# Kernel tuning notes

Measured on AMD Instinct MI355X. Metric: run time of the kernel, lower is better.

The kernel has to match this reference:

```python
import jax, jax.numpy as jnp
import numpy as np

B, S, D_IN, D_H, D_OUT = 32, 1024, 512, 512, 512
N_HEADS, K_NEI = 2, 3
LN_EPS = 1e-5


def _layernorm(x, g, b):
    mu = x.mean(-1, keepdims=True)
    xc = x - mu
    var = (xc * xc).mean(-1, keepdims=True)
    return xc * jax.lax.rsqrt(var + LN_EPS) * g + b


def setup_inputs() -> dict:
    key = jax.random.key(0)
    ks = jax.random.split(key, 8)
    sc = 0.02
    rn = lambda k, shape: jax.random.normal(k, shape, jnp.float32) * sc
    return {
        "x": jax.random.normal(ks[0], (B, S, D_IN), jnp.float32),
        "enc_w": rn(ks[1], (D_H, D_IN)), "enc_b": jnp.zeros((D_H,), jnp.float32),
        "in_w": rn(ks[2], (3 * D_H, D_H)), "in_b": jnp.zeros((3 * D_H,), jnp.float32),
        "out_w": rn(ks[3], (D_H, D_H)), "out_b": jnp.zeros((D_H,), jnp.float32),
        "ln1_g": jnp.ones((D_H,), jnp.float32), "ln1_b": jnp.zeros((D_H,), jnp.float32),
        "ffn_w1": rn(ks[4], (2 * D_H, D_H)), "ffn_b1": jnp.zeros((2 * D_H,), jnp.float32),
        "ffn_w2": rn(ks[5], (D_H, 2 * D_H)), "ffn_b2": jnp.zeros((D_H,), jnp.float32),
        "gc_w": rn(ks[6], (D_H, 2 * D_H)), "gc_b": jnp.zeros((D_H,), jnp.float32),
        "ln2_g": jnp.ones((D_H,), jnp.float32), "ln2_b": jnp.zeros((D_H,), jnp.float32),
        "dec_w": rn(ks[7], (D_OUT, D_H)), "dec_b": jnp.zeros((D_OUT,), jnp.float32),
    }


def reference(x, enc_w, enc_b, in_w, in_b, out_w, out_b, ln1_g, ln1_b,
              ffn_w1, ffn_b1, ffn_w2, ffn_b2, gc_w, gc_b, ln2_g, ln2_b,
              dec_w, dec_b):
    # --- encoder ---
    h = jax.nn.relu(x @ enc_w.T + enc_b)                          # [B,S,Dh]

    # --- ElevateH0toH1: self-attention + LN + residual FFN ---
    qkv = h @ in_w.T + in_b                                       # [B,S,3Dh]
    q, k, v = jnp.split(qkv, 3, axis=-1)
    dh = D_H // N_HEADS
    heads = lambda t: t.reshape(B, S, N_HEADS, dh).transpose(0, 2, 1, 3)
    q, k, v = heads(q), heads(k), heads(v)
    scores = jnp.einsum("bhqd,bhkd->bhqk", q, k) / jnp.sqrt(jnp.float32(dh))
    attn = jax.nn.softmax(scores, axis=-1)
    ctx = jnp.einsum("bhqk,bhkd->bhqd", attn, v)
    ctx = ctx.transpose(0, 2, 1, 3).reshape(B, S, D_H)
    attn_out = ctx @ out_w.T + out_b
    x1 = _layernorm(h + attn_out, ln1_g, ln1_b)
    x1 = x1 + (jax.nn.relu(x1 @ ffn_w1.T + ffn_b1) @ ffn_w2.T + ffn_b2)

    # --- ElevateH1toH2: symmetric KNN adjacency from cosine similarity ---
    nrm = x1 / jnp.maximum(jnp.linalg.norm(x1, axis=-1, keepdims=True), 1e-12)
    sim = jnp.einsum("bid,bjd->bij", nrm, nrm)                    # [B,S,S]
    kk = min(K_NEI, S - 1)
    _, idx = jax.lax.top_k(sim, kk + 1)                           # [B,S,k+1] (incl. self)
    mask = jnp.zeros((B, S, S), bool).at[
        jnp.arange(B)[:, None, None], jnp.arange(S)[None, :, None], idx
    ].set(True)
    mask = mask & ~jnp.eye(S, dtype=bool)                         # drop self edges
    mask = mask | mask.transpose(0, 2, 1)                         # symmetrize
    adj = jnp.where(mask, sim, jnp.float32(0.0))

    nsum = jnp.einsum("bij,bjd->bid", adj, x1)
    cnt = jnp.maximum(adj.sum(-1, keepdims=True), jnp.float32(1.0))
    combined = jnp.concatenate([x1, nsum / cnt], axis=-1)         # [B,S,2Dh]
    out = combined @ gc_w.T + gc_b
    x2 = _layernorm(x1 + out, ln2_g, ln2_b)

    # --- pool + decoder ---
    return x2.mean(axis=1) @ dec_w.T + dec_b                      # [B,D_OUT]
```

## Files before the change

kernel.cpp:

```cpp
#include <hip/hip_runtime.h>
#include <hip/hip_bf16.h>
#include <math.h>

typedef unsigned short u16;
typedef __attribute__((ext_vector_type(8))) short bfrag;
typedef __attribute__((ext_vector_type(4))) float facc;
typedef const __attribute__((address_space(1))) void* gaddr_t;
typedef __attribute__((address_space(3))) void* laddr_t;

#define F_RELU   1
#define F_ROWSC  4
#define F_SIMSC  8
#define F_RESID2 32

__device__ __forceinline__ u16 f2bf(float f) {
  __hip_bfloat16 h = __float2bfloat16(f);
  return *reinterpret_cast<u16*>(&h);
}
__device__ __forceinline__ float bf2f(u16 u) {
  __hip_bfloat16 h = *reinterpret_cast<__hip_bfloat16*>(&u);
  return __bfloat162float(h);
}
__device__ __forceinline__ float wsum(float v) {
#pragma unroll
  for (int o = 32; o; o >>= 1) v += __shfl_xor(v, o);
  return v;
}
__device__ __forceinline__ float wmaxf(float v) {
#pragma unroll
  for (int o = 32; o; o >>= 1) v = fmaxf(v, __shfl_xor(v, o));
  return v;
}

struct GSeg {
  const u16* A; const u16* B;
  long sA, sB;
  int lda, ldb, K;
  int hA, hB;
};

__global__ __launch_bounds__(256)
void bgemm_k(GSeg s0, GSeg s1, GSeg s2,
             const float* __restrict__ bias,
             const u16* __restrict__ residH, const u16* __restrict__ residL,
             const float* __restrict__ rsc, const float* __restrict__ csc,
             float* __restrict__ Cf, u16* __restrict__ Cb, u16* __restrict__ Cb2,
             int ldc, long sC, int hC, int headBits, int sS,
             float alpha, int flags, int Mstore)
{
  const int zAll = blockIdx.z;
  const int hIdx = headBits ? (zAll & 1) : 0;
  const int z    = headBits ? (zAll >> 1) : zAll;
  const long cofs = (long)z * sC + (long)hIdx * hC;
  const float* rs = rsc ? rsc + (long)z * sS : nullptr;
  const float* cs = csc ? csc + (long)z * sS : nullptr;

  __shared__ u16 As[2][128 * 64];
  __shared__ u16 Bs[2][128 * 64];

  const int tid  = threadIdx.x;
  const int wave = tid >> 6, lane = tid & 63;
  const int m0 = blockIdx.x * 128, n0 = blockIdx.y * 128;
  const int wrow = (wave >> 1) * 64, wcol = (wave & 1) * 64;

  const u16* ApS[3]; const u16* BpS[3]; int ldaS[3], ldbS[3];
  ApS[0] = s0.A + (long)z * s0.sA + (long)hIdx * s0.hA;
  BpS[0] = s0.B + (long)z * s0.sB + (long)hIdx * s0.hB;
  ldaS[0] = s0.lda; ldbS[0] = s0.ldb;
  ApS[1] = s1.A ? s1.A + (long)z * s1.sA + (long)hIdx * s1.hA : nullptr;
  BpS[1] = s1.B ? s1.B + (long)z * s1.sB + (long)hIdx * s1.hB : nullptr;
  ldaS[1] = s1.lda; ldbS[1] = s1.ldb;
  ApS[2] = s2.A ? s2.A + (long)z * s2.sA + (long)hIdx * s2.hA : nullptr;
  BpS[2] = s2.B ? s2.B + (long)z * s2.sB + (long)hIdx * s2.hB : nullptr;
  ldaS[2] = s2.lda; ldbS[2] = s2.ldb;
  const int n0i = s0.K >> 6, n1i = n0i + (s1.K >> 6);
  const int nIt = n1i + (s2.K >> 6);

  const int lrow = lane >> 3;
  const int lgrp = lane & 7;

  facc acc[4][4];
#pragma unroll
  for (int i = 0; i < 4; ++i)
#pragma unroll
    for (int j = 0; j < 4; ++j) acc[i][j] = (facc)(0.f);

  const int r16 = lane & 15, gq = lane >> 4;

  auto stage = [&](int buf, int it) {
    int sidx, base;
    if (it < n0i)      { sidx = 0; base = 0; }
    else if (it < n1i) { sidx = 1; base = n0i; }
    else               { sidx = 2; base = n1i; }
    const int k0 = (it - base) << 6;
    const u16* Ab = ApS[sidx];
    const u16* Bb = BpS[sidx];
    const int la = ldaS[sidx], lb = ldbS[sidx];
#pragma unroll
    for (int ss = 0; ss < 4; ++ss) {
      int rloc = wave * 32 + ss * 8;
      int row  = rloc + lrow;
      int g    = lgrp ^ ((row >> 1) & 7);
      __builtin_amdgcn_global_load_lds(
          (gaddr_t)(const void*)(Ab + (long)(m0 + row) * la + k0 + g * 8),
          (laddr_t)(As[buf] + rloc * 64), 16, 0, 0);
      __builtin_amdgcn_global_load_lds(
          (gaddr_t)(const void*)(Bb + (long)(n0 + row) * lb + k0 + g * 8),
          (laddr_t)(Bs[buf] + rloc * 64), 16, 0, 0);
    }
  };

  stage(0, 0);
  for (int it = 0; it < nIt; ++it) {
    const int buf = it & 1;
    __syncthreads();
    if (it + 1 < nIt) stage(buf ^ 1, it + 1);

#pragma unroll
    for (int kk = 0; kk < 2; ++kk) {
      bfrag af[4], bb[4];
#pragma unroll
      for (int mt = 0; mt < 4; ++mt) {
        int r = wrow + mt * 16 + r16;
        int slot = (kk * 4 + gq) ^ ((r >> 1) & 7);
        af[mt] = *(const bfrag*)&As[buf][r * 64 + slot * 8];
      }
#pragma unroll
      for (int nt = 0; nt < 4; ++nt) {
        int r = wcol + nt * 16 + r16;
        int slot = (kk * 4 + gq) ^ ((r >> 1) & 7);
        bb[nt] = *(const bfrag*)&Bs[buf][r * 64 + slot * 8];
      }
#pragma unroll
      for (int mt = 0; mt < 4; ++mt)
#pragma unroll
        for (int nt = 0; nt < 4; ++nt)
          acc[mt][nt] = __builtin_amdgcn_mfma_f32_16x16x32_bf16(
              af[mt], bb[nt], acc[mt][nt], 0, 0, 0);
    }
  }

#pragma unroll
  for (int mt = 0; mt < 4; ++mt) {
#pragma unroll
    for (int nt = 0; nt < 4; ++nt) {
#pragma unroll
      for (int r = 0; r < 4; ++r) {
        int gm = m0 + wrow + mt * 16 + gq * 4 + r;
        int gn = n0 + wcol + nt * 16 + r16;
        if (gm >= Mstore) continue;
        float v = acc[mt][nt][r] * alpha;
        long ci = cofs + (long)gm * ldc + gn;
        if (flags & F_SIMSC)  v *= rs[gm] * cs[gn];
        if (flags & F_ROWSC)  v *= rs[gm];
        if (bias)             v += bias[gn];
        if (flags & F_RESID2) v += bf2f(residH[ci]) + bf2f(residL[ci]);
        if (flags & F_RELU)   v = fmaxf(v, 0.f);
        if (Cf) Cf[ci] = v;
        if (Cb) {
          u16 hv = f2bf(v);
          Cb[ci] = hv;
          if (Cb2) Cb2[ci] = f2bf(v - bf2f(hv));
        }
      }
    }
  }
}

__global__ __launch_bounds__(256)
void castbf_k(const float* __restrict__ in, u16* __restrict__ out, int n)
{
  int i = blockIdx.x * 256 + threadIdx.x;
  if (i < n) out[i] = f2bf(in[i]);
}

__global__ __launch_bounds__(256)
void castw_k(const float* w0, const float* w1, const float* w2,
             const float* w3, const float* w4, const float* w5,
             const float* w6, u16* __restrict__ dst)
{
  int i = blockIdx.x * 256 + threadIdx.x;
  const float* s; int off;
  if      (i < 262144)  { s = w0; off = 0; }
  else if (i < 1048576) { s = w1; off = 262144; }
  else if (i < 1310720) { s = w2; off = 1048576; }
  else if (i < 1835008) { s = w3; off = 1310720; }
  else if (i < 2359296) { s = w4; off = 1835008; }
  else if (i < 2883584) { s = w5; off = 2359296; }
  else                  { s = w6; off = 2883584; }
  dst[i] = f2bf(s[i - off]);
}

__global__ __launch_bounds__(256)
void ln1_k(const u16* __restrict__ a, const u16* __restrict__ b,
           const float* __restrict__ g, const float* __restrict__ be,
           u16* __restrict__ oh, u16* __restrict__ ol)
{
  long base = (long)blockIdx.x * 512;
  int t = threadIdx.x;
  float v0 = bf2f(a[base + t])       + bf2f(b[base + t]);
  float v1 = bf2f(a[base + t + 256]) + bf2f(b[base + t + 256]);
  __shared__ float red[4], red2[4];
  float s = wsum(v0 + v1);
  if ((t & 63) == 0) red[t >> 6] = s;
  __syncthreads();
  float mean = (red[0] + red[1] + red[2] + red[3]) * (1.f / 512.f);
  float c0 = v0 - mean, c1 = v1 - mean;
  float ss = wsum(c0 * c0 + c1 * c1);
  if ((t & 63) == 0) red2[t >> 6] = ss;
  __syncthreads();
  float var = (red2[0] + red2[1] + red2[2] + red2[3]) * (1.f / 512.f);
  float rstd = rsqrtf(var + 1e-5f);
  float o0 = c0 * rstd * g[t]       + be[t];
  float o1 = c1 * rstd * g[t + 256] + be[t + 256];
  u16 h0 = f2bf(o0), h1 = f2bf(o1);
  oh[base + t] = h0;       oh[base + t + 256] = h1;
  ol[base + t] = f2bf(o0 - bf2f(h0));
  ol[base + t + 256] = f2bf(o1 - bf2f(h1));
}

__global__ __launch_bounds__(256)
void ln2_k(const u16* __restrict__ hi, const u16* __restrict__ lo,
           const u16* __restrict__ b, const float* __restrict__ g,
           const float* __restrict__ be, u16* __restrict__ ob)
{
  long base = (long)blockIdx.x * 512;
  int t = threadIdx.x;
  float v0 = bf2f(hi[base + t])       + bf2f(lo[base + t])       + bf2f(b[base + t]);
  float v1 = bf2f(hi[base + t + 256]) + bf2f(lo[base + t + 256]) + bf2f(b[base + t + 256]);
  __shared__ float red[4], red2[4];
  float s = wsum(v0 + v1);
  if ((t & 63) == 0) red[t >> 6] = s;
  __syncthreads();
  float mean = (red[0] + red[1] + red[2] + red[3]) * (1.f / 512.f);
  float c0 = v0 - mean, c1 = v1 - mean;
  float ss = wsum(c0 * c0 + c1 * c1);
  if ((t & 63) == 0) red2[t >> 6] = ss;
  __syncthreads();
  float var = (red2[0] + red2[1] + red2[2] + red2[3]) * (1.f / 512.f);
  float rstd = rsqrtf(var + 1e-5f);
  ob[base + t]       = f2bf(c0 * rstd * g[t]       + be[t]);
  ob[base + t + 256] = f2bf(c1 * rstd * g[t + 256] + be[t + 256]);
}

__global__ __launch_bounds__(256)
void rownorm_k(const u16* __restrict__ hi, const u16* __restrict__ lo,
               float* __restrict__ invn)
{
  long base = (long)blockIdx.x * 512;
  int t = threadIdx.x;
  float v0 = bf2f(hi[base + t])       + bf2f(lo[base + t]);
  float v1 = bf2f(hi[base + t + 256]) + bf2f(lo[base + t + 256]);
  __shared__ float red[4];
  float s = wsum(v0 * v0 + v1 * v1);
  if ((t & 63) == 0) red[t >> 6] = s;
  __syncthreads();
  if (t == 0) {
    float tot = red[0] + red[1] + red[2] + red[3];
    invn[blockIdx.x] = 1.f / fmaxf(sqrtf(tot), 1e-12f);
  }
}

__global__ __launch_bounds__(256)
void softmaxu_k(u16* __restrict__ sc)
{
  long row = blockIdx.x;
  u16* p = sc + row * 1024;
  int t = threadIdx.x;
  float v[4];
#pragma unroll
  for (int i = 0; i < 4; ++i) v[i] = bf2f(p[t + 256 * i]);
  __shared__ float redm[4], redsum[4];
  float m4 = fmaxf(fmaxf(v[0], v[1]), fmaxf(v[2], v[3]));
  float wm = wmaxf(m4);
  if ((t & 63) == 0) redm[t >> 6] = wm;
  __syncthreads();
  float MX = fmaxf(fmaxf(redm[0], redm[1]), fmaxf(redm[2], redm[3]));
  float s = 0.f;
#pragma unroll
  for (int i = 0; i < 4; ++i) { v[i] = __expf(v[i] - MX); s += v[i]; }
  float ws_ = wsum(s);
  if ((t & 63) == 0) redsum[t >> 6] = ws_;
  __syncthreads();
  float inv = 1.f / (redsum[0] + redsum[1] + redsum[2] + redsum[3]);
#pragma unroll
  for (int i = 0; i < 4; ++i) p[t + 256 * i] = f2bf(v[i] * inv);
}

__global__ __launch_bounds__(256)
void transp_k(const u16* __restrict__ in, u16* __restrict__ out,
              int inStride, int outStride, long sIn, long sOut,
              int hIn, int headBits)
{
  const int zAll = blockIdx.z;
  const int h  = headBits ? (zAll & 1) : 0;
  const int zb = headBits ? (zAll >> 1) : zAll;
  const u16* src = in + (long)zb * sIn + (long)h * hIn;
  u16* dst = out + (long)zAll * sOut;
  const int r0 = blockIdx.x * 64, c0 = blockIdx.y * 64;
  __shared__ u16 tile[64][66];
  const int t = threadIdx.x;
#pragma unroll
  for (int p = 0; p < 16; ++p) {
    int idx = p * 256 + t;
    int r = idx >> 6, c = idx & 63;
    tile[r][c] = src[(long)(r0 + r) * inStride + c0 + c];
  }
  __syncthreads();
#pragma unroll
  for (int p = 0; p < 16; ++p) {
    int idx = p * 256 + t;
    int c = idx >> 6, r = idx & 63;
    dst[(long)(c0 + c) * outStride + r0 + r] = tile[r][c];
  }
}

__global__ __launch_bounds__(64)
void topk_k(const float* __restrict__ sim, int* __restrict__ idx4)
{
  long row = blockIdx.x;
  const float* p = sim + row * 1024;
  int t = threadIdx.x;
  int c0 = -1, c1 = -1, c2 = -1, c3 = -1;
#pragma unroll
  for (int pass = 0; pass < 4; ++pass) {
    float best = -INFINITY;
    int bi = 1 << 30;
    for (int j = t; j < 1024; j += 64) {
      if (j == c0 || j == c1 || j == c2 || j == c3) continue;
      float v = p[j];
      if (v > best || (v == best && j < bi)) { best = v; bi = j; }
    }
#pragma unroll
    for (int off = 32; off; off >>= 1) {
      float ov = __shfl_down(best, off);
      int   oi = __shfl_down(bi, off);
      if (ov > best || (ov == best && oi < bi)) { best = ov; bi = oi; }
    }
    bi = __shfl(bi, 0);
    if (pass == 0) c0 = bi; else if (pass == 1) c1 = bi;
    else if (pass == 2) c2 = bi; else c3 = bi;
  }
  if (t == 0) { int* q = idx4 + row * 4; q[0] = c0; q[1] = c1; q[2] = c2; q[3] = c3; }
}

__global__ __launch_bounds__(256)
void adjbf_k(const float* __restrict__ sim, const int* __restrict__ idx4,
             u16* __restrict__ adjb, float* __restrict__ invcnt)
{
  long row = blockIdx.x;
  int b = (int)(row >> 10);
  int i = (int)(row & 1023);
  const float* prow = sim + row * 1024;
  u16* arow_ = adjb + row * 1024;
  const int* my = idx4 + row * 4;
  int m0 = my[0], m1 = my[1], m2 = my[2], m3 = my[3];
  int t = threadIdx.x;
  float lsum = 0.f;
  for (int j = t; j < 1024; j += 256) {
    float v = prow[j];
    bool present = false;
    if (j != i) {
      present = (j == m0) | (j == m1) | (j == m2) | (j == m3);
      if (!present) {
        const int* oj = idx4 + (((long)b << 10) + j) * 4;
        present = (oj[0] == i) | (oj[1] == i) | (oj[2] == i) | (oj[3] == i);
      }
    }
    float a = present ? v : 0.f;
    arow_[j] = f2bf(a);
    lsum += a;
  }
  __shared__ float red[4];
  float s = wsum(lsum);
  if ((t & 63) == 0) red[t >> 6] = s;
  __syncthreads();
  if (t == 0) {
    float tot = red[0] + red[1] + red[2] + red[3];
    invcnt[row] = 1.f / fmaxf(tot, 1.f);
  }
}

__global__ __launch_bounds__(256)
void poolbf_k(const u16* __restrict__ x2, u16* __restrict__ pooled)
{
  int i = blockIdx.x * 256 + threadIdx.x;
  int b = i >> 9, d = i & 511;
  float s = 0.f;
  if (b < 32) {
    const u16* p = x2 + ((long)b << 10) * 512 + d;
    for (int sdx = 0; sdx < 1024; ++sdx) s += bf2f(p[(long)sdx * 512]);
    s *= (1.f / 1024.f);
  }
  pooled[i] = f2bf(s);
}

static inline GSeg mkseg(const u16* A, const u16* B, int K, int lda, int ldb,
                         long sA = 0, long sB = 0, int hA = 0, int hB = 0)
{
  GSeg s; s.A = A; s.B = B; s.K = K; s.lda = lda; s.ldb = ldb;
  s.sA = sA; s.sB = sB; s.hA = hA; s.hB = hB; return s;
}

static inline void bgemm(hipStream_t st, GSeg s0, GSeg s1, GSeg s2,
    const float* bias, const u16* residH, const u16* residL,
    const float* rsc, const float* csc, float* Cf, u16* Cb, u16* Cb2,
    int M, int N, int ldc, long sC, int hC, int headBits, int sS,
    float alpha, int flags, int nz, int Mstore = -1)
{
  dim3 g(M / 128, N / 128, nz);
  bgemm_k<<<g, 256, 0, st>>>(s0, s1, s2, bias, residH, residL,
                             rsc, csc, Cf, Cb, Cb2, ldc, sC, hC, headBits,
                             sS, alpha, flags, Mstore < 0 ? M : Mstore);
}

extern "C" void kernel_launch(void* const* d_in, const int* in_sizes, int n_in,
                              void* d_out, int out_size, void* d_ws, size_t ws_size,
                              hipStream_t stream)
{
  (void)in_sizes; (void)n_in; (void)out_size;
  const float* x     = (const float*)d_in[0];
  const float* enc_w = (const float*)d_in[1];
  const float* enc_b = (const float*)d_in[2];
  const float* in_w  = (const float*)d_in[3];
  const float* in_b  = (const float*)d_in[4];
  const float* out_w = (const float*)d_in[5];
  const float* out_b = (const float*)d_in[6];
  const float* ln1_g = (const float*)d_in[7];
  const float* ln1_b = (const float*)d_in[8];
  const float* fw1   = (const float*)d_in[9];
  const float* fb1   = (const float*)d_in[10];
  const float* fw2   = (const float*)d_in[11];
  const float* fb2   = (const float*)d_in[12];
  const float* gc_w  = (const float*)d_in[13];
  const float* gc_b  = (const float*)d_in[14];
  const float* ln2_g = (const float*)d_in[15];
  const float* ln2_b = (const float*)d_in[16];
  const float* dec_w = (const float*)d_in[17];
  const float* dec_b = (const float*)d_in[18];
  float* out = (float*)d_out;

  char* base = (char*)d_ws;
  u16*  bf1  = (u16*)(base);
  u16*  lob  = (u16*)(base + 33554432);
  u16*  bf2  = (u16*)(base + 67108864);
  u16*  wgt  = (u16*)(base + 100663296);
  float* invn    = (float*)(base + 106954752);
  float* invcnt  = (float*)(base + 107085824);
  u16*   pooledb = (u16*)(base + 107216896);
  int*   idx4    = (int*)(base + 107347968);
  char*  scr     = base + 107872256;
  const size_t need = 107872256 + 83886080;
  if (ws_size < need) return;

  u16* encw = wgt;
  u16* inw  = wgt + 262144;
  u16* outw = wgt + 1048576;
  u16* fw1b = wgt + 1310720;
  u16* fw2b = wgt + 1835008;
  u16* gcwb = wgt + 2359296;
  u16* decw = wgt + 2883584;

  const int Mtok = 32768;
  GSeg Z = mkseg(nullptr, nullptr, 0, 0, 0);

  u16* xbf = (u16*)scr;
  castbf_k<<<65536, 256, 0, stream>>>(x, xbf, 16777216);
  castw_k<<<12288, 256, 0, stream>>>(enc_w, in_w, out_w, fw1, fw2, gc_w, dec_w, wgt);

  bgemm(stream, mkseg(xbf, encw, 512, 512, 512), Z, Z,
        enc_b, nullptr, nullptr, nullptr, nullptr, nullptr, bf1, nullptr,
        Mtok, 512, 512, 0, 0, 0, 0, 1.f, F_RELU, 1);

  for (int c = 0; c < 4; ++c) {
    long row0 = (long)c * 8192;
    u16* qkvc = (u16*)scr;
    u16* sco  = (u16*)(scr + 25165824);
    u16* vT   = (u16*)(scr + 58720256);
    bgemm(stream, mkseg(bf1 + row0 * 512, inw, 512, 512, 512), Z, Z,
          in_b, nullptr, nullptr, nullptr, nullptr, nullptr, qkvc, nullptr,
          8192, 1536, 1536, 0, 0, 0, 0, 1.f, 0, 1);
    bgemm(stream, mkseg(qkvc, qkvc + 512, 256, 1536, 1536,
                        1572864, 1572864, 256, 256), Z, Z,
          nullptr, nullptr, nullptr, nullptr, nullptr, nullptr, sco, nullptr,
          1024, 1024, 1024, 2097152, 1048576, 1, 0, 0.0625f, 0, 16);
    softmaxu_k<<<16384, 256, 0, stream>>>(sco);
    transp_k<<<dim3(16, 4, 16), 256, 0, stream>>>(
        qkvc + 1024, vT, 1536, 1024, 1572864, 262144, 256, 1);
    bgemm(stream, mkseg(sco, vT, 1024, 1024, 1024,
                        2097152, 524288, 1048576, 262144), Z, Z,
          nullptr, nullptr, nullptr, nullptr, nullptr, nullptr,
          bf2 + row0 * 512, nullptr,
          1024, 256, 512, 524288, 256, 1, 0, 1.f, 0, 16);
  }

  u16* aoc = (u16*)scr;
  bgemm(stream, mkseg(bf2, outw, 512, 512, 512), Z, Z,
        out_b, nullptr, nullptr, nullptr, nullptr, nullptr, aoc, nullptr,
        Mtok, 512, 512, 0, 0, 0, 0, 1.f, 0, 1);

  ln1_k<<<Mtok, 256, 0, stream>>>(bf1, aoc, ln1_g, ln1_b, bf1, lob);

  u16* mid = (u16*)scr;
  bgemm(stream, mkseg(bf1, fw1b, 512, 512, 512), Z, Z,
        fb1, nullptr, nullptr, nullptr, nullptr, nullptr, mid, nullptr,
        Mtok, 1024, 1024, 0, 0, 0, 0, 1.f, F_RELU, 1);
  bgemm(stream, mkseg(mid, fw2b, 1024, 1024, 1024), Z, Z,
        fb2, bf1, lob, nullptr, nullptr, nullptr, bf1, lob,
        Mtok, 512, 512, 0, 0, 0, 0, 1.f, F_RESID2, 1);

  rownorm_k<<<Mtok, 256, 0, stream>>>(bf1, lob, invn);

  float* simc = (float*)scr;
  u16*   adjb = (u16*)(scr + 33554432);
  u16*   x1T  = (u16*)(scr + 50331648);
  transp_k<<<dim3(16, 8, 32), 256, 0, stream>>>(bf1, x1T, 512, 1024,
                                                524288, 524288, 0, 0);
  for (int g = 0; g < 4; ++g) {
    long row0 = (long)g * 8192;
    bgemm(stream,
          mkseg(bf1 + row0 * 512, bf1 + row0 * 512, 512, 512, 512, 524288, 524288),
          Z, Z, nullptr, nullptr, nullptr, invn + row0, invn + row0,
          simc, nullptr, nullptr,
          1024, 1024, 1024, 1048576, 0, 0, 1024, 1.f, F_SIMSC, 8);
    topk_k<<<8192, 64, 0, stream>>>(simc, idx4 + row0 * 4);
    adjbf_k<<<8192, 256, 0, stream>>>(simc, idx4 + row0 * 4, adjb, invcnt + row0);
    bgemm(stream, mkseg(adjb, x1T + row0 * 512, 1024, 1024, 1024,
                        1048576, 524288), Z, Z,
          nullptr, nullptr, nullptr, invcnt + row0, nullptr, nullptr,
          bf2 + row0 * 512, nullptr,
          1024, 512, 512, 524288, 0, 0, 1024, 1.f, F_ROWSC, 8);
  }

  u16* gch = (u16*)scr;
  bgemm(stream, mkseg(bf1, gcwb, 512, 512, 1024),
        mkseg(bf2, gcwb + 512, 512, 512, 1024), Z,
        gc_b, nullptr, nullptr, nullptr, nullptr, nullptr, gch, nullptr,
        Mtok, 512, 512, 0, 0, 0, 0, 1.f, 0, 1);

  ln2_k<<<Mtok, 256, 0, stream>>>(bf1, lob, gch, ln2_g, ln2_b, bf2);

  poolbf_k<<<256, 256, 0, stream>>>(bf2, pooledb);
  bgemm(stream, mkseg(pooledb, decw, 512, 512, 512), Z, Z,
        dec_b, nullptr, nullptr, nullptr, nullptr, out, nullptr, nullptr,
        128, 512, 512, 0, 0, 0, 0, 1.f, 0, 1, 32);
}
```

Measured before the change: 1.605 ms.

## Store similarity in bf16, mask adjacency in place, batch 16 per group

The cosine-similarity GEMM now writes bf16 instead of fp32. The adjacency kernel zeroes non-neighbours in place in that same buffer, so the separate fp32 sim and bf16 adj buffers are gone. Top-k is rewritten as a 256-thread block that stages the row in shared memory and reduces across waves. With the smaller footprint the per-group batch count doubles from 8 to 16, halving the number of launches. The aim is to cut HBM traffic and launch overhead, at the cost that top-k now ranks bf16-rounded similarities, which can change tie-breaking and neighbour selection relative to fp32.

```diff
diff --git a/kernel.cpp b/kernel.cpp
--- a/kernel.cpp
+++ b/kernel.cpp
@@ -315,20 +315,27 @@
   }
 }
 
-__global__ __launch_bounds__(64)
-void topk_k(const float* __restrict__ sim, int* __restrict__ idx4)
-{
-  long row = blockIdx.x;
-  const float* p = sim + row * 1024;
+__global__ __launch_bounds__(256)
+void topk_k(const u16* __restrict__ sim, int* __restrict__ idx4)
+{
+  __shared__ float row[1024];
+  __shared__ float bv[4];
+  __shared__ int   bidx[4];
+  long r = blockIdx.x;
+  const u16* p = sim + r * 1024;
   int t = threadIdx.x;
+  for (int i = t; i < 1024; i += 256) row[i] = bf2f(p[i]);
+  __syncthreads();
   int c0 = -1, c1 = -1, c2 = -1, c3 = -1;
 #pragma unroll
   for (int pass = 0; pass < 4; ++pass) {
     float best = -INFINITY;
     int bi = 1 << 30;
-    for (int j = t; j < 1024; j += 64) {
+#pragma unroll
+    for (int q = 0; q < 4; ++q) {
+      int j = t + q * 256;
       if (j == c0 || j == c1 || j == c2 || j == c3) continue;
-      float v = p[j];
+      float v = row[j];
       if (v > best || (v == best && j < bi)) { best = v; bi = j; }
     }
 #pragma unroll
@@ -337,28 +344,38 @@
       int   oi = __shfl_down(bi, off);
       if (ov > best || (ov == best && oi < bi)) { best = ov; bi = oi; }
     }
-    bi = __shfl(bi, 0);
-    if (pass == 0) c0 = bi; else if (pass == 1) c1 = bi;
-    else if (pass == 2) c2 = bi; else c3 = bi;
-  }
-  if (t == 0) { int* q = idx4 + row * 4; q[0] = c0; q[1] = c1; q[2] = c2; q[3] = c3; }
-}
-
-__global__ __launch_bounds__(256)
-void adjbf_k(const float* __restrict__ sim, const int* __restrict__ idx4,
-             u16* __restrict__ adjb, float* __restrict__ invcnt)
+    if ((t & 63) == 0) { bv[t >> 6] = best; bidx[t >> 6] = bi; }
+    __syncthreads();
+    if (t == 0) {
+      float bb = bv[0]; int ii = bidx[0];
+#pragma unroll
+      for (int w = 1; w < 4; ++w)
+        if (bv[w] > bb || (bv[w] == bb && bidx[w] < ii)) { bb = bv[w]; ii = bidx[w]; }
+      bidx[0] = ii;
+    }
+    __syncthreads();
+    int sel = bidx[0];
+    if (pass == 0) c0 = sel; else if (pass == 1) c1 = sel;
+    else if (pass == 2) c2 = sel; else c3 = sel;
+    __syncthreads();
+  }
+  if (t == 0) { int* q = idx4 + r * 4; q[0] = c0; q[1] = c1; q[2] = c2; q[3] = c3; }
+}
+
+__global__ __launch_bounds__(256)
+void adjbf_k(u16* __restrict__ simadj, const int* __restrict__ idx4,
+             float* __restrict__ invcnt)
 {
   long row = blockIdx.x;
   int b = (int)(row >> 10);
   int i = (int)(row & 1023);
-  const float* prow = sim + row * 1024;
-  u16* arow_ = adjb + row * 1024;
+  u16* prow = simadj + row * 1024;
   const int* my = idx4 + row * 4;
   int m0 = my[0], m1 = my[1], m2 = my[2], m3 = my[3];
   int t = threadIdx.x;
   float lsum = 0.f;
   for (int j = t; j < 1024; j += 256) {
-    float v = prow[j];
+    float v = bf2f(prow[j]);
     bool present = false;
     if (j != i) {
       present = (j == m0) | (j == m1) | (j == m2) | (j == m3);
@@ -368,7 +385,7 @@
       }
     }
     float a = present ? v : 0.f;
-    arow_[j] = f2bf(a);
+    prow[j] = present ? prow[j] : (u16)0;
     lsum += a;
   }
   __shared__ float red[4];
@@ -511,25 +528,24 @@
 
   rownorm_k<<<Mtok, 256, 0, stream>>>(bf1, lob, invn);
 
-  float* simc = (float*)scr;
-  u16*   adjb = (u16*)(scr + 33554432);
-  u16*   x1T  = (u16*)(scr + 50331648);
+  u16* simadj = (u16*)scr;
+  u16* x1T    = (u16*)(scr + 33554432);
   transp_k<<<dim3(16, 8, 32), 256, 0, stream>>>(bf1, x1T, 512, 1024,
                                                 524288, 524288, 0, 0);
-  for (int g = 0; g < 4; ++g) {
-    long row0 = (long)g * 8192;
+  for (int g = 0; g < 2; ++g) {
+    long row0 = (long)g * 16384;
     bgemm(stream,
           mkseg(bf1 + row0 * 512, bf1 + row0 * 512, 512, 512, 512, 524288, 524288),
           Z, Z, nullptr, nullptr, nullptr, invn + row0, invn + row0,
-          simc, nullptr, nullptr,
-          1024, 1024, 1024, 1048576, 0, 0, 1024, 1.f, F_SIMSC, 8);
-    topk_k<<<8192, 64, 0, stream>>>(simc, idx4 + row0 * 4);
-    adjbf_k<<<8192, 256, 0, stream>>>(simc, idx4 + row0 * 4, adjb, invcnt + row0);
-    bgemm(stream, mkseg(adjb, x1T + row0 * 512, 1024, 1024, 1024,
+          nullptr, simadj, nullptr,
+          1024, 1024, 1024, 1048576, 0, 0, 1024, 1.f, F_SIMSC, 16);
+    topk_k<<<16384, 256, 0, stream>>>(simadj, idx4 + row0 * 4);
+    adjbf_k<<<16384, 256, 0, stream>>>(simadj, idx4 + row0 * 4, invcnt + row0);
+    bgemm(stream, mkseg(simadj, x1T + row0 * 512, 1024, 1024, 1024,
                         1048576, 524288), Z, Z,
           nullptr, nullptr, nullptr, invcnt + row0, nullptr, nullptr,
           bf2 + row0 * 512, nullptr,
-          1024, 512, 512, 524288, 0, 0, 1024, 1.f, F_ROWSC, 8);
+          1024, 512, 512, 524288, 0, 0, 1024, 1.f, F_ROWSC, 16);
   }
 
   u16* gch = (u16*)scr;
```

Result: faster. 1.534 ms (-4.4%).
